# Kernel tuning notes

Hardware: AMD Instinct MI355X
Metric: run time of the kernel (lower is better)

## Reference

```python
import jax, jax.numpy as jnp
import numpy as np

B, N, DIM, H, DH, K = 2, 2048, 1024, 8, 64, 32
INNER = H * DH  # 512


def setup_inputs() -> dict:
    key = jax.random.key(0)
    ks = jax.random.split(key, 10)
    x = jax.random.normal(ks[0], (B, N, DIM), dtype=jnp.float32)
    # retrieved memories: b (h n) j kv d, already l2-normalized in the original pipeline
    mem_kv = jax.random.normal(ks[1], (B, H * N, K, 2, DH), dtype=jnp.float32)
    mem_kv = mem_kv / jnp.linalg.norm(mem_kv, axis=-1, keepdims=True)
    mem_mask = jnp.ones((B, H * N, K), dtype=bool)
    s = 0.02
    Wq = jax.random.normal(ks[2], (DIM, INNER), dtype=jnp.float32) * s
    Wkv = jax.random.normal(ks[3], (DIM, 2 * DH), dtype=jnp.float32) * s
    Wo = jax.random.normal(ks[4], (INNER, DIM), dtype=jnp.float32) * s
    bo = jnp.zeros((DIM,), dtype=jnp.float32)
    null_k = jax.random.normal(ks[5], (DH,), dtype=jnp.float32)
    null_v = jax.random.normal(ks[6], (DH,), dtype=jnp.float32)
    gate = jax.random.normal(ks[7], (H, 1, 1), dtype=jnp.float32)
    return dict(x=x, Wq=Wq, Wkv=Wkv, Wo=Wo, bo=bo, null_k=null_k,
                null_v=null_v, gate=gate, mem_kv=mem_kv, mem_mask=mem_mask)


def reference(x, Wq, Wkv, Wo, bo, null_k, null_v, gate, mem_kv, mem_mask):
    b, n, _ = x.shape
    scale = DH ** -0.5
    neg = -jnp.finfo(x.dtype).max

    q = (x @ Wq).reshape(b, n, H, DH).transpose(0, 2, 1, 3)  # b h n d
    kv = x @ Wkv                                             # b n 2d (single kv head)
    k, v = kv[..., :DH], kv[..., DH:]

    # local causal attention: full n x n scores
    sim = jnp.einsum('bhid,bjd->bhij', q, k) * scale
    causal = jnp.triu(jnp.ones((n, n), dtype=bool), 1)
    sim = jnp.where(causal, neg, sim)
    attn = jax.nn.softmax(sim, axis=-1)
    local_values = jnp.einsum('bhij,bjd->bhid', attn, v)    # b h n d

    # memory branch: per-query gathered keys/values + null slot
    mk = mem_kv[..., 0, :].reshape(b, H, n, K, DH)           # b h i j d
    mv = mem_kv[..., 1, :].reshape(b, H, n, K, DH)
    mmask = mem_mask.reshape(b, H, n, K)
    nk = jnp.broadcast_to(null_k, (b, H, n, 1, DH))
    nv = jnp.broadcast_to(null_v, (b, H, n, 1, DH))
    mk = jnp.concatenate([nk, mk], axis=-2)                  # b h i (1+j) d
    mv = jnp.concatenate([nv, mv], axis=-2)
    mmask = jnp.concatenate([jnp.ones((b, H, n, 1), dtype=bool), mmask], axis=-1)

    sim_mem = jnp.einsum('bhid,bhijd->bhij', q, mk) * scale
    sim_mem = jnp.where(mmask, sim_mem, neg)
    attn_mem = jax.nn.softmax(sim_mem, axis=-1)
    mem_values = jnp.einsum('bhij,bhijd->bhid', attn_mem, mv)

    g = jax.nn.sigmoid(gate)                                 # h 1 1 -> broadcast
    out = local_values * g + mem_values * (1.0 - g)          # b h n d
    out = out.transpose(0, 2, 1, 3).reshape(b, n, INNER)
    return out @ Wo + bo
```

## Files before the change

kernel.cpp:

```cpp
#include <hip/hip_runtime.h>

typedef unsigned short u16;
typedef unsigned int u32;
typedef __attribute__((ext_vector_type(8))) short short8;
typedef __attribute__((ext_vector_type(4))) float f32x4;

#define BB 2
#define NN 2048
#define DIMD 1024
#define HH 8
#define DH 64
#define INNER 512

__device__ __forceinline__ u16 f2bf(float f) {
    u32 u = __builtin_bit_cast(u32, f);
    u32 r = (u + 0x7fffu + ((u >> 16) & 1u)) >> 16;
    return (u16)r;
}
__device__ __forceinline__ float bf2f(u16 b) {
    u32 u = ((u32)b) << 16;
    return __builtin_bit_cast(float, u);
}

__global__ __launch_bounds__(256) void k0t(
    const float* __restrict__ Wq, const float* __restrict__ Wkv, const float* __restrict__ Wo,
    u16* __restrict__ WT, u16* __restrict__ WoT)
{
    __shared__ float tl[64][65];
    int bid = blockIdx.x, t = threadIdx.x;
    const float* src; u16* dst; int C, Kdim, r0, c0, drb; float sc;
    if (bid < 128)       { src = Wq;  dst = WT;  C = 512;  Kdim = 1024; r0 = (bid >> 3) * 64;          c0 = (bid & 7) * 64;          drb = 0;   sc = 0.125f; }
    else if (bid < 160)  { int q = bid - 128; src = Wkv; dst = WT;  C = 128;  Kdim = 1024; r0 = (q >> 1) * 64; c0 = (q & 1) * 64;  drb = 512; sc = 1.f; }
    else                 { int q = bid - 160; src = Wo;  dst = WoT; C = 1024; Kdim = 512;  r0 = (q >> 4) * 64; c0 = (q & 15) * 64; drb = 0;   sc = 1.f; }
    int c = t & 63, rr = t >> 6;
    #pragma unroll
    for (int i = 0; i < 16; i++) {
        int r = i * 4 + rr;
        tl[r][c] = src[(size_t)(r0 + r) * C + c0 + c];
    }
    __syncthreads();
    #pragma unroll
    for (int i = 0; i < 16; i++) {
        int n = i * 4 + rr;
        dst[(size_t)(drb + c0 + n) * Kdim + r0 + c] = f2bf(tl[c][n] * sc);
    }
}

__global__ __launch_bounds__(256) void k1_proj(
    const float* __restrict__ x, const u16* __restrict__ WT,
    u16* __restrict__ qb, u16* __restrict__ kb, u16* __restrict__ vT)
{
    __shared__ u16 As[64][72];
    __shared__ u16 Bs[64][72];
    int bid = blockIdx.x;
    int mblk = bid / 10, nblk = bid - mblk * 10;
    int mt0 = mblk * 64, nt0 = nblk * 64;
    int t = threadIdx.x;
    int w = t >> 6, l = t & 63;
    int lr = l & 15, lg = l >> 4;
    int srow = t >> 2, scol = (t & 3) * 16;
    const float* Axs = x + (size_t)(mt0 + srow) * DIMD + scol;
    const u16* Bsrc = WT + (size_t)(nt0 + srow) * DIMD + scol;
    f32x4 acc[4];
    #pragma unroll
    for (int i = 0; i < 4; i++) acc[i] = (f32x4){0.f, 0.f, 0.f, 0.f};
    f32x4 xa[4]; uint4 b0, b1;
    #pragma unroll
    for (int j = 0; j < 4; j++) xa[j] = *(const f32x4*)(Axs + 4 * j);
    b0 = *(const uint4*)(Bsrc); b1 = *(const uint4*)(Bsrc + 8);
    for (int kc = 0; kc < DIMD; kc += 64) {
        u16 apk[16];
        #pragma unroll
        for (int j = 0; j < 4; j++)
            #pragma unroll
            for (int cc = 0; cc < 4; cc++) apk[j * 4 + cc] = f2bf(xa[j][cc]);
        __syncthreads();
        *(uint4*)&As[srow][scol]     = *(const uint4*)&apk[0];
        *(uint4*)&As[srow][scol + 8] = *(const uint4*)&apk[8];
        *(uint4*)&Bs[srow][scol]     = b0;
        *(uint4*)&Bs[srow][scol + 8] = b1;
        __syncthreads();
        if (kc + 64 < DIMD) {
            #pragma unroll
            for (int j = 0; j < 4; j++) xa[j] = *(const f32x4*)(Axs + kc + 64 + 4 * j);
            b0 = *(const uint4*)(Bsrc + kc + 64); b1 = *(const uint4*)(Bsrc + kc + 72);
        }
        #pragma unroll
        for (int kt = 0; kt < 64; kt += 32) {
            short8 af = *(const short8*)&As[w * 16 + lr][kt + lg * 8];
            #pragma unroll
            for (int nc = 0; nc < 4; nc++) {
                short8 bf = *(const short8*)&Bs[nc * 16 + lr][kt + lg * 8];
                acc[nc] = __builtin_amdgcn_mfma_f32_16x16x32_bf16(af, bf, acc[nc], 0, 0, 0);
            }
        }
    }
    #pragma unroll
    for (int nc = 0; nc < 4; nc++) {
        #pragma unroll
        for (int r = 0; r < 4; r++) {
            int col = nt0 + 16 * nc + lr;
            int row = mt0 + w * 16 + lg * 4 + r;
            int b = row >> 11, i = row & 2047;
            u16 bits = f2bf(acc[nc][r]);
            if (col < INNER) {
                int h = col >> 6, d = col & 63;
                qb[(((size_t)(b * HH + h)) * NN + i) * DH + d] = bits;
            } else if (col < INNER + DH) {
                kb[((size_t)b * NN + i) * DH + (col - INNER)] = bits;
            } else {
                vT[((size_t)b * DH + (col - INNER - DH)) * NN + i] = bits;
            }
        }
    }
}

__global__ __launch_bounds__(256, 5) void k2_fused(
    const u16* __restrict__ qb, const u16* __restrict__ kb, const u16* __restrict__ vT,
    const float* __restrict__ mem_kv, const float* __restrict__ null_k, const float* __restrict__ null_v,
    float* __restrict__ loc_o, float* __restrict__ mem_o)
{
    __shared__ union {
        u16 pl[4][16 * 72];
        struct {
            float accs[4][16][64];
            float ml0[4][16];
            float ml1[4][16];
        } c;
    } sh;
    int bid = blockIdx.x;
    int w = threadIdx.x >> 6, l = threadIdx.x & 63;

    if ((bid & 1) == 0) {
        int mw = (bid >> 1) * 4 + w;
        int g = l >> 4, m = l & 15;
        f32x4 nk4 = *(const f32x4*)(null_k + 4 * m);
        f32x4 nv4 = *(const f32x4*)(null_v + 4 * m);
        for (int t = 0; t < 4; t++) {
            int r = mw * 4 + t;
            const float* rowp = mem_kv + (size_t)r * 4096;
            f32x4 K[8], V[8];
            #pragma unroll
            for (int i = 0; i < 8; i++) {
                const float* sp = rowp + (size_t)(4 * i + g) * 128 + 4 * m;
                K[i] = __builtin_nontemporal_load((const f32x4*)sp);
                V[i] = __builtin_nontemporal_load((const f32x4*)(sp + 64));
            }
            uint2 qw = *(const uint2*)(qb + (size_t)r * 64 + 4 * m);
            float q0 = bf2f((u16)qw.x), q1 = bf2f((u16)(qw.x >> 16));
            float q2 = bf2f((u16)qw.y), q3 = bf2f((u16)(qw.y >> 16));
            float sims[8];
            #pragma unroll
            for (int i = 0; i < 8; i++) {
                float p = K[i][0] * q0 + K[i][1] * q1 + K[i][2] * q2 + K[i][3] * q3;
                p += __shfl_xor(p, 1); p += __shfl_xor(p, 2);
                p += __shfl_xor(p, 4); p += __shfl_xor(p, 8);
                sims[i] = p;
            }
            float sn = nk4[0] * q0 + nk4[1] * q1 + nk4[2] * q2 + nk4[3] * q3;
            sn += __shfl_xor(sn, 1); sn += __shfl_xor(sn, 2);
            sn += __shfl_xor(sn, 4); sn += __shfl_xor(sn, 8);
            float mx = fmaxf(fmaxf(fmaxf(sims[0], sims[1]), fmaxf(sims[2], sims[3])),
                             fmaxf(fmaxf(sims[4], sims[5]), fmaxf(sims[6], sims[7])));
            mx = fmaxf(mx, __shfl_xor(mx, 16));
            mx = fmaxf(mx, __shfl_xor(mx, 32));
            mx = fmaxf(mx, sn);
            float den = 0.f;
            f32x4 acc = {0.f, 0.f, 0.f, 0.f};
            #pragma unroll
            for (int i = 0; i < 8; i++) {
                float e = __expf(sims[i] - mx);
                den += e;
                acc[0] += e * V[i][0]; acc[1] += e * V[i][1];
                acc[2] += e * V[i][2]; acc[3] += e * V[i][3];
            }
            den += __shfl_xor(den, 16); den += __shfl_xor(den, 32);
            float en = __expf(sn - mx);
            den += en;
            float inv = 1.f / den;
            #pragma unroll
            for (int c = 0; c < 4; c++) {
                acc[c] += __shfl_xor(acc[c], 16);
                acc[c] += __shfl_xor(acc[c], 32);
                acc[c] = (acc[c] + en * nv4[c]) * inv;
            }
            if (g == 0)
                *(float4*)(mem_o + (size_t)r * 64 + 4 * m) = make_float4(acc[0], acc[1], acc[2], acc[3]);
        }
    } else {
        int li = bid >> 1;
        int bh = li & 15, tIdx = li >> 4;
        int it16 = (tIdx & 1) ? (127 - (tIdx >> 1)) : (tIdx >> 1);
        int it = it16 << 4;
        int b = bh >> 3, h = bh & 7;
        int lr = l & 15, lg = l >> 4;
        const u16* qrow = qb + (((size_t)(b * HH + h)) * NN + it + lr) * DH;
        short8 qa0 = *(const short8*)(qrow + lg * 8);
        short8 qa1 = *(const short8*)(qrow + 32 + lg * 8);
        f32x4 acc[4];
        #pragma unroll
        for (int i = 0; i < 4; i++) acc[i] = (f32x4){0.f, 0.f, 0.f, 0.f};
        float m = -3e38f;
        float lsum = 0.f;
        int T = (it >> 6) + 1;
        u16* plw = &sh.pl[w][0];
        const f32x4 z4 = {0.f, 0.f, 0.f, 0.f};
        for (int ji = w; ji < T; ji += 4) {
            int jt = ji * 64;
            f32x4 st[4];
            #pragma unroll
            for (int nc = 0; nc < 4; nc++) {
                const u16* kr = kb + ((size_t)b * NN + jt + 16 * nc + lr) * DH;
                short8 k0 = *(const short8*)(kr + lg * 8);
                short8 k1 = *(const short8*)(kr + 32 + lg * 8);
                f32x4 t2 = __builtin_amdgcn_mfma_f32_16x16x32_bf16(k0, qa0, z4, 0, 0, 0);
                st[nc] = __builtin_amdgcn_mfma_f32_16x16x32_bf16(k1, qa1, t2, 0, 0, 0);
            }
            if (ji == T - 1) {
                #pragma unroll
                for (int nc = 0; nc < 4; nc++)
                    #pragma unroll
                    for (int r = 0; r < 4; r++) {
                        int j = jt + 16 * nc + lg * 4 + r;
                        if (j > it + lr) st[nc][r] = -3e38f;
                    }
            }
            float pm = st[0][0];
            #pragma unroll
            for (int nc = 0; nc < 4; nc++)
                #pragma unroll
                for (int r = 0; r < 4; r++) pm = fmaxf(pm, st[nc][r]);
            if (!__all(pm <= m + 8.f)) {
                float rm = fmaxf(pm, __shfl_xor(pm, 16));
                rm = fmaxf(rm, __shfl_xor(rm, 32));
                float mnew = fmaxf(m, rm);
                float fs = __expf(m - mnew);
                float fr[4];
                #pragma unroll
                for (int r = 0; r < 4; r++) fr[r] = __shfl(fs, lg * 4 + r);
                #pragma unroll
                for (int nc = 0; nc < 4; nc++) {
                    acc[nc][0] *= fr[0]; acc[nc][1] *= fr[1];
                    acc[nc][2] *= fr[2]; acc[nc][3] *= fr[3];
                }
                lsum *= fs;
                m = mnew;
            }
            #pragma unroll
            for (int nc = 0; nc < 4; nc++) {
                float p0 = __expf(st[nc][0] - m);
                float p1 = __expf(st[nc][1] - m);
                float p2 = __expf(st[nc][2] - m);
                float p3 = __expf(st[nc][3] - m);
                lsum += (p0 + p1) + (p2 + p3);
                u32 w0 = (u32)f2bf(p0) | ((u32)f2bf(p1) << 16);
                u32 w1 = (u32)f2bf(p2) | ((u32)f2bf(p3) << 16);
                *(uint2*)&plw[lr * 72 + 16 * nc + 4 * lg] = make_uint2(w0, w1);
            }
            short8 pa0 = *(const short8*)(plw + lr * 72 + lg * 8);
            short8 pa1 = *(const short8*)(plw + lr * 72 + 32 + lg * 8);
            #pragma unroll
            for (int nc = 0; nc < 4; nc++) {
                const u16* vp = vT + ((size_t)b * DH + 16 * nc + lr) * NN + jt;
                short8 v0 = *(const short8*)(vp + lg * 8);
                short8 v1 = *(const short8*)(vp + 32 + lg * 8);
                f32x4 t2 = __builtin_amdgcn_mfma_f32_16x16x32_bf16(pa0, v0, acc[nc], 0, 0, 0);
                acc[nc] = __builtin_amdgcn_mfma_f32_16x16x32_bf16(pa1, v1, t2, 0, 0, 0);
            }
        }
        lsum += __shfl_xor(lsum, 16);
        lsum += __shfl_xor(lsum, 32);
        __syncthreads();
        #pragma unroll
        for (int nc = 0; nc < 4; nc++)
            #pragma unroll
            for (int r = 0; r < 4; r++)
                sh.c.accs[w][lg * 4 + r][16 * nc + lr] = acc[nc][r];
        if (lg == 0) {
            sh.c.ml0[w][lr] = m;
            sh.c.ml1[w][lr] = lsum;
        }
        __syncthreads();
        #pragma unroll
        for (int r = 0; r < 4; r++) {
            int row = lg * 4 + r;
            float m0 = sh.c.ml0[0][row], m1 = sh.c.ml0[1][row];
            float m2 = sh.c.ml0[2][row], m3 = sh.c.ml0[3][row];
            float mt = fmaxf(fmaxf(m0, m1), fmaxf(m2, m3));
            float f0 = __expf(m0 - mt), f1 = __expf(m1 - mt);
            float f2 = __expf(m2 - mt), f3 = __expf(m3 - mt);
            float lt = f0 * sh.c.ml1[0][row] + f1 * sh.c.ml1[1][row]
                     + f2 * sh.c.ml1[2][row] + f3 * sh.c.ml1[3][row];
            float o = f0 * sh.c.accs[0][row][16 * w + lr] + f1 * sh.c.accs[1][row][16 * w + lr]
                    + f2 * sh.c.accs[2][row][16 * w + lr] + f3 * sh.c.accs[3][row][16 * w + lr];
            loc_o[(((size_t)(b * HH + h)) * NN + it + row) * DH + 16 * w + lr] = o / lt;
        }
    }
}

__global__ __launch_bounds__(256) void k3_out(
    const float* __restrict__ loc_o, const float* __restrict__ mem_o,
    const float* __restrict__ gate, const u16* __restrict__ WoT,
    const float* __restrict__ bo, float* __restrict__ out)
{
    __shared__ u16 As[64][72];
    __shared__ u16 Bs[64][72];
    int bid = blockIdx.x;
    int mblk = bid >> 4, nblk = bid & 15;
    int mt0 = mblk * 64, nt0 = nblk * 64;
    int t = threadIdx.x;
    int w = t >> 6, l = t & 63;
    int lr = l & 15, lg = l >> 4;
    int srow = t >> 2, scol = (t & 3) * 16;
    int arow = mt0 + srow;
    int ab = arow >> 11, ai = arow & 2047;
    const float* lbase = loc_o + ((size_t)(ab * HH) * NN + ai) * DH;
    const float* mbase = mem_o + ((size_t)(ab * HH) * NN + ai) * DH;
    const u16* Bsrc = WoT + (size_t)(nt0 + srow) * INNER + scol;
    f32x4 acc[4];
    #pragma unroll
    for (int i = 0; i < 4; i++) acc[i] = (f32x4){0.f, 0.f, 0.f, 0.f};

    for (int kc = 0; kc < INNER; kc += 64) {
        int h = kc >> 6;
        float gh = 1.f / (1.f + __expf(-gate[h]));
        size_t off = (size_t)h * (NN * DH) + scol;
        f32x4 lv[4], mv[4];
        #pragma unroll
        for (int j = 0; j < 4; j++) {
            lv[j] = *(const f32x4*)(lbase + off + 4 * j);
            mv[j] = *(const f32x4*)(mbase + off + 4 * j);
        }
        uint4 b0 = *(const uint4*)(Bsrc + kc);
        uint4 b1 = *(const uint4*)(Bsrc + kc + 8);
        u16 apk[16];
        #pragma unroll
        for (int j = 0; j < 4; j++) {
            #pragma unroll
            for (int c = 0; c < 4; c++)
                apk[j * 4 + c] = f2bf(lv[j][c] * gh + mv[j][c] * (1.f - gh));
        }
        __syncthreads();
        *(uint4*)&As[srow][scol]     = *(const uint4*)&apk[0];
        *(uint4*)&As[srow][scol + 8] = *(const uint4*)&apk[8];
        *(uint4*)&Bs[srow][scol]     = b0;
        *(uint4*)&Bs[srow][scol + 8] = b1;
        __syncthreads();
        #pragma unroll
        for (int kt = 0; kt < 64; kt += 32) {
            short8 af = *(const short8*)&As[w * 16 + lr][kt + lg * 8];
            #pragma unroll
            for (int nc = 0; nc < 4; nc++) {
                short8 bf = *(const short8*)&Bs[nc * 16 + lr][kt + lg * 8];
                acc[nc] = __builtin_amdgcn_mfma_f32_16x16x32_bf16(af, bf, acc[nc], 0, 0, 0);
            }
        }
    }
    #pragma unroll
    for (int nc = 0; nc < 4; nc++) {
        int col = nt0 + 16 * nc + lr;
        float bv = bo[col];
        #pragma unroll
        for (int r = 0; r < 4; r++) {
            int row = mt0 + w * 16 + lg * 4 + r;
            out[(size_t)row * DIMD + col] = acc[nc][r] + bv;
        }
    }
}

extern "C" void kernel_launch(void* const* d_in, const int* in_sizes, int n_in,
                              void* d_out, int out_size, void* d_ws, size_t ws_size,
                              hipStream_t stream) {
    const float* x      = (const float*)d_in[0];
    const float* Wq     = (const float*)d_in[1];
    const float* Wkv    = (const float*)d_in[2];
    const float* Wo     = (const float*)d_in[3];
    const float* bo     = (const float*)d_in[4];
    const float* null_k = (const float*)d_in[5];
    const float* null_v = (const float*)d_in[6];
    const float* gate   = (const float*)d_in[7];
    const float* mem_kv = (const float*)d_in[8];
    float* out = (float*)d_out;

    char* ws = (char*)d_ws;
    u16*  WT      = (u16*)(ws);
    u16*  WoT     = (u16*)(ws + 1310720);
    u16*  qb      = (u16*)(ws + 2359296);
    u16*  kb      = (u16*)(ws + 6553600);
    u16*  vT      = (u16*)(ws + 7077888);
    float* mem_o  = (float*)(ws + 7602176);
    float* loc_o  = (float*)(ws + 15990784);

    hipLaunchKernelGGL(k0t,      dim3(288),  dim3(256), 0, stream, Wq, Wkv, Wo, WT, WoT);
    hipLaunchKernelGGL(k1_proj,  dim3(640),  dim3(256), 0, stream, x, WT, qb, kb, vT);
    hipLaunchKernelGGL(k2_fused, dim3(4096), dim3(256), 0, stream, qb, kb, vT, mem_kv, null_k, null_v, loc_o, mem_o);
    hipLaunchKernelGGL(k3_out,   dim3(1024), dim3(256), 0, stream, loc_o, mem_o, gate, WoT, bo, out);
}
```

Before: 199.1 us.

## Split gate combine into separate bf16 kernel and prefetch tiles in output GEMM

Moves the sigmoid-gated blend of local and memory outputs out of the output projection into a new elementwise kernel. That kernel writes a bf16 token-major activation. The output GEMM then loads compact bf16 tiles instead of re-reading two fp32 tensors once per N-block, and it prefetches the next K tile into registers before the MFMA loop. The cost is an extra kernel launch plus an extra write and read of the combined activation.

```diff
diff --git a/kernel.cpp b/kernel.cpp
--- a/kernel.cpp
+++ b/kernel.cpp
@@ -298,9 +298,27 @@
     }
 }
 
+__global__ __launch_bounds__(256) void k2_combine(
+    const float* __restrict__ loc_o, const float* __restrict__ mem_o,
+    const float* __restrict__ gate, u16* __restrict__ av)
+{
+    int t = blockIdx.x * 256 + threadIdx.x;
+    int idx = t * 2;
+    int d = idx & 63;
+    int i = (idx >> 6) & 2047;
+    int h = (idx >> 17) & 7;
+    int b = idx >> 20;
+    float2 lv = *(const float2*)(loc_o + idx);
+    float2 mv = *(const float2*)(mem_o + idx);
+    float g = 1.f / (1.f + __expf(-gate[h]));
+    float r0 = lv.x * g + mv.x * (1.f - g);
+    float r1 = lv.y * g + mv.y * (1.f - g);
+    u32 packed = (u32)f2bf(r0) | ((u32)f2bf(r1) << 16);
+    *(u32*)(av + ((size_t)(b * NN + i)) * INNER + h * DH + d) = packed;
+}
+
 __global__ __launch_bounds__(256) void k3_out(
-    const float* __restrict__ loc_o, const float* __restrict__ mem_o,
-    const float* __restrict__ gate, const u16* __restrict__ WoT,
+    const u16* __restrict__ av, const u16* __restrict__ WoT,
     const float* __restrict__ bo, float* __restrict__ out)
 {
     __shared__ u16 As[64][72];
@@ -312,40 +330,23 @@
     int w = t >> 6, l = t & 63;
     int lr = l & 15, lg = l >> 4;
     int srow = t >> 2, scol = (t & 3) * 16;
-    int arow = mt0 + srow;
-    int ab = arow >> 11, ai = arow & 2047;
-    const float* lbase = loc_o + ((size_t)(ab * HH) * NN + ai) * DH;
-    const float* mbase = mem_o + ((size_t)(ab * HH) * NN + ai) * DH;
+    const u16* Asrc = av + (size_t)(mt0 + srow) * INNER + scol;
     const u16* Bsrc = WoT + (size_t)(nt0 + srow) * INNER + scol;
     f32x4 acc[4];
     #pragma unroll
     for (int i = 0; i < 4; i++) acc[i] = (f32x4){0.f, 0.f, 0.f, 0.f};
-
+    uint4 a0, a1, b0, b1;
+    a0 = *(const uint4*)(Asrc); a1 = *(const uint4*)(Asrc + 8);
+    b0 = *(const uint4*)(Bsrc); b1 = *(const uint4*)(Bsrc + 8);
     for (int kc = 0; kc < INNER; kc += 64) {
-        int h = kc >> 6;
-        float gh = 1.f / (1.f + __expf(-gate[h]));
-        size_t off = (size_t)h * (NN * DH) + scol;
-        f32x4 lv[4], mv[4];
-        #pragma unroll
-        for (int j = 0; j < 4; j++) {
-            lv[j] = *(const f32x4*)(lbase + off + 4 * j);
-            mv[j] = *(const f32x4*)(mbase + off + 4 * j);
-        }
-        uint4 b0 = *(const uint4*)(Bsrc + kc);
-        uint4 b1 = *(const uint4*)(Bsrc + kc + 8);
-        u16 apk[16];
-        #pragma unroll
-        for (int j = 0; j < 4; j++) {
-            #pragma unroll
-            for (int c = 0; c < 4; c++)
-                apk[j * 4 + c] = f2bf(lv[j][c] * gh + mv[j][c] * (1.f - gh));
-        }
-        __syncthreads();
-        *(uint4*)&As[srow][scol]     = *(const uint4*)&apk[0];
-        *(uint4*)&As[srow][scol + 8] = *(const uint4*)&apk[8];
-        *(uint4*)&Bs[srow][scol]     = b0;
-        *(uint4*)&Bs[srow][scol + 8] = b1;
-        __syncthreads();
+        __syncthreads();
+        *(uint4*)&As[srow][scol] = a0;  *(uint4*)&As[srow][scol + 8] = a1;
+        *(uint4*)&Bs[srow][scol] = b0;  *(uint4*)&Bs[srow][scol + 8] = b1;
+        __syncthreads();
+        if (kc + 64 < INNER) {
+            a0 = *(const uint4*)(Asrc + kc + 64); a1 = *(const uint4*)(Asrc + kc + 72);
+            b0 = *(const uint4*)(Bsrc + kc + 64); b1 = *(const uint4*)(Bsrc + kc + 72);
+        }
         #pragma unroll
         for (int kt = 0; kt < 64; kt += 32) {
             short8 af = *(const short8*)&As[w * 16 + lr][kt + lg * 8];
@@ -390,9 +391,11 @@
     u16*  vT      = (u16*)(ws + 7077888);
     float* mem_o  = (float*)(ws + 7602176);
     float* loc_o  = (float*)(ws + 15990784);
-
-    hipLaunchKernelGGL(k0t,      dim3(288),  dim3(256), 0, stream, Wq, Wkv, Wo, WT, WoT);
-    hipLaunchKernelGGL(k1_proj,  dim3(640),  dim3(256), 0, stream, x, WT, qb, kb, vT);
-    hipLaunchKernelGGL(k2_fused, dim3(4096), dim3(256), 0, stream, qb, kb, vT, mem_kv, null_k, null_v, loc_o, mem_o);
-    hipLaunchKernelGGL(k3_out,   dim3(1024), dim3(256), 0, stream, loc_o, mem_o, gate, WoT, bo, out);
-}
+    u16*  av      = (u16*)(ws + 24379392);
+
+    hipLaunchKernelGGL(k0t,        dim3(288),  dim3(256), 0, stream, Wq, Wkv, Wo, WT, WoT);
+    hipLaunchKernelGGL(k1_proj,    dim3(640),  dim3(256), 0, stream, x, WT, qb, kb, vT);
+    hipLaunchKernelGGL(k2_fused,   dim3(4096), dim3(256), 0, stream, qb, kb, vT, mem_kv, null_k, null_v, loc_o, mem_o);
+    hipLaunchKernelGGL(k2_combine, dim3(4096), dim3(256), 0, stream, loc_o, mem_o, gate, av);
+    hipLaunchKernelGGL(k3_out,     dim3(1024), dim3(256), 0, stream, av, WoT, bo, out);
+}
```

New measurement: 184.4 us, median of 2. 1.08x faster.
